# Kernel tuning notes

Hardware: AMD Instinct MI355X
Metric: run time of the kernel (lower is better)

The kernel has to match this reference:

```python
import jax, jax.numpy as jnp
import numpy as np

N_NODES = 50000
N_EDGES = 800000
EMB = 128
N_LAYERS = 2
BN_EPS = 1e-5


def setup_inputs() -> dict:
    key = jax.random.key(0)
    ks = jax.random.split(key, 16)
    N, E, D, L = N_NODES, N_EDGES, EMB, N_LAYERS
    x = jax.random.randint(ks[0], (N, 2), 0, 3)
    edge_index = jax.random.randint(ks[1], (2, E), 0, N)
    edge_attr = jax.random.randint(ks[2], (E, 2), 0, 3)
    batch = jnp.zeros((N,), dtype=jnp.int32)
    s = 0.1
    xemb1 = jax.random.normal(ks[3], (120, D)) * s   # atom-type embedding
    xemb2 = jax.random.normal(ks[4], (3, D)) * s     # chirality embedding
    e1 = jax.random.normal(ks[5], (L, 7, D)) * s     # bond-type embedding per layer
    e2 = jax.random.normal(ks[6], (L, 3, D)) * s     # bond-direction embedding per layer
    W1 = jax.random.normal(ks[7], (L, D, 2 * D)) * s
    b1 = jnp.zeros((L, 2 * D))
    W2 = jax.random.normal(ks[8], (L, 2 * D, D)) * s
    b2 = jnp.zeros((L, D))
    gamma = jnp.ones((L, D))
    beta = jnp.zeros((L, D))
    return {"x": x, "edge_index": edge_index, "edge_attr": edge_attr, "batch": batch,
            "xemb1": xemb1, "xemb2": xemb2, "e1": e1, "e2": e2,
            "W1": W1, "b1": b1, "W2": W2, "b2": b2, "gamma": gamma, "beta": beta}


def _gnn_forward(x, edge_index, edge_attr, xemb1, xemb2, e1, e2, W1, b1, W2, b2, gamma, beta):
    N = x.shape[0]
    # add self loops; self-loop edge_attr = [4, 0]
    loop = jnp.arange(N, dtype=edge_index.dtype)
    src = jnp.concatenate([edge_index[0], loop])
    dst = jnp.concatenate([edge_index[1], loop])
    loop_attr = jnp.concatenate([jnp.full((N, 1), 4, dtype=edge_attr.dtype),
                                 jnp.zeros((N, 1), dtype=edge_attr.dtype)], axis=1)
    ea = jnp.concatenate([edge_attr, loop_attr], axis=0)  # [E+N, 2]

    # input node embedding
    h = xemb1[x[:, 0]] + xemb2[x[:, 1]]  # [N, D]

    for l in range(N_LAYERS):
        eemb = e1[l][ea[:, 0]] + e2[l][ea[:, 1]]      # [E+N, D]
        msg = h[src] + eemb                            # gather + edge fuse
        agg = jax.ops.segment_sum(msg, dst, num_segments=N)  # scatter-add
        # GIN update MLP: Linear -> ReLU -> Linear
        h2 = jax.nn.relu(agg @ W1[l] + b1[l]) @ W2[l] + b2[l]
        # BatchNorm1d (training mode: biased batch stats)
        mu = jnp.mean(h2, axis=0)
        var = jnp.mean(jnp.square(h2 - mu), axis=0)
        h2 = gamma[l] * (h2 - mu) * jax.lax.rsqrt(var + BN_EPS) + beta[l]
        # dropout(relu) for non-final layers; drop_ratio=0 -> identity dropout
        h = h2 if l == N_LAYERS - 1 else jax.nn.relu(h2)
    return h  # JK='last'


def reference(x, edge_index, edge_attr, batch, xemb1, xemb2, e1, e2, W1, b1, W2, b2, gamma, beta):
    return _gnn_forward(x, edge_index, edge_attr, xemb1, xemb2, e1, e2, W1, b1, W2, b2, gamma, beta)
```

## Files before the change

kernel.cpp:

```cpp
#include <hip/hip_runtime.h>
#include <stdint.h>

#define N_NODES 50000
#define N_EDGES 800000
#define EMB 128
#define NPAD 50176
#define MBLK 392
#define BN_EPS 1e-5f
#define SENT_KEY ((N_NODES << 5) | 21)
#define NODES_PER_XCD 6250
#define XCHUNK 2048
#define NCHUNKS ((N_EDGES + XCHUNK - 1) / XCHUNK)
#define PBLK 196

typedef __attribute__((ext_vector_type(8))) short short8;
typedef __attribute__((ext_vector_type(4))) float f32x4;

__device__ __forceinline__ unsigned short f2bf(float f) {
    unsigned int u = __float_as_uint(f);
    u += 0x7fffu + ((u >> 16) & 1u);
    return (unsigned short)(u >> 16);
}
__device__ __forceinline__ float bflo(unsigned int v) { return __uint_as_float(v << 16); }
__device__ __forceinline__ float bfhi(unsigned int v) { return __uint_as_float(v & 0xffff0000u); }
__device__ __forceinline__ unsigned int packbf(float lo, float hi) {
    return (unsigned int)f2bf(lo) | ((unsigned int)f2bf(hi) << 16);
}

__global__ void k_prep(const int* __restrict__ x, const float* __restrict__ xe1,
                       const float* __restrict__ xe2, unsigned int* __restrict__ h,
                       const float* __restrict__ W1, const float* __restrict__ W2,
                       unsigned short* __restrict__ w1t, unsigned short* __restrict__ w2t,
                       int* __restrict__ deg,
                       const int* __restrict__ ei, const int* __restrict__ ea,
                       int* __restrict__ keyv, float* __restrict__ bnsum,
                       int* __restrict__ bmeta) {
    int idx = blockIdx.x * 256 + threadIdx.x;
    int i = idx >> 6, j = idx & 63;
    if (i < N_NODES) {
        int a = x[2 * i], c = x[2 * i + 1];
        float2 va = *(const float2*)(xe1 + a * EMB + j * 2);
        float2 vb = *(const float2*)(xe2 + c * EMB + j * 2);
        h[i * 64 + j] = packbf(va.x + vb.x, va.y + vb.y);
    } else if (i == N_NODES) {
        h[(size_t)i * 64 + j] = 0u;
    }
    if (idx < 4 * 32768) {
        int sec = idx >> 15, q = idx & 32767;
        if (sec < 2) {
            int r = q >> 8, c = q & 255;
            w1t[sec * 32768 + c * 128 + r] = f2bf(W1[sec * 32768 + q]);
        } else {
            int s = sec - 2;
            int r = q >> 7, c = q & 127;
            w2t[s * 32768 + c * 256 + r] = f2bf(W2[s * 32768 + q]);
        }
    }
    if (idx < N_EDGES) {
        int2 aa = *(const int2*)(ea + 2 * idx);
        keyv[idx] = (ei[idx] << 5) | (aa.x * 3 + aa.y);
    }
    if (idx < N_NODES) deg[idx] = 0;
    if (idx < 512) bnsum[idx] = 0.f;
    if (idx < 16) bmeta[idx] = 0;
}

__global__ void k_hist(const int* __restrict__ dst, int* __restrict__ deg) {
    int xcd = blockIdx.x & 7, chunk = blockIdx.x >> 3;
    int lo = xcd * NODES_PER_XCD, hi = lo + NODES_PER_XCD;
    int e0 = chunk * XCHUNK + threadIdx.x * 4;
#pragma unroll
    for (int it = 0; it < XCHUNK / 1024; ++it) {
        int e = e0 + it * 1024;
        if (e < N_EDGES) {
            int4 d4 = *(const int4*)(dst + e);
            if (d4.x >= lo && d4.x < hi) atomicAdd(&deg[d4.x], 1);
            if (d4.y >= lo && d4.y < hi) atomicAdd(&deg[d4.y], 1);
            if (d4.z >= lo && d4.z < hi) atomicAdd(&deg[d4.z], 1);
            if (d4.w >= lo && d4.w < hi) atomicAdd(&deg[d4.w], 1);
        }
    }
}

__global__ void k_scan1(const int* __restrict__ deg, int* __restrict__ part, int* __restrict__ bsums) {
    __shared__ int wsum[16];
    int lane = threadIdx.x & 63, wid = threadIdx.x >> 6;
    int i = blockIdx.x * 1024 + threadIdx.x;
    int d = (i < N_NODES) ? deg[i] : 0;
    int v = (d + 15) & ~15;
    int s = v;
#pragma unroll
    for (int off = 1; off < 64; off <<= 1) {
        int t = __shfl_up(s, off);
        if (lane >= off) s += t;
    }
    if (lane == 63) wsum[wid] = s;
    __syncthreads();
    if (wid == 0) {
        int w = (lane < 16) ? wsum[lane] : 0;
#pragma unroll
        for (int off = 1; off < 16; off <<= 1) {
            int t = __shfl_up(w, off);
            if (lane >= off) w += t;
        }
        if (lane < 16) wsum[lane] = w;
    }
    __syncthreads();
    int base = (wid > 0) ? wsum[wid - 1] : 0;
    if (i < N_NODES) part[i] = base + s - v;
    if (threadIdx.x == 1023) bsums[blockIdx.x] = wsum[15];
}

__global__ void k_scan3(const int* __restrict__ part, const int* __restrict__ bsums,
                        const int* __restrict__ deg, int* __restrict__ offs,
                        int* __restrict__ cursor, int* __restrict__ keys,
                        int* __restrict__ bcnt) {
    __shared__ int bs[64];
    __shared__ int lc[8];
    int tid = threadIdx.x;
    if (tid < 8) lc[tid] = 0;
    if (tid < 64) {
        int v = (tid < 49) ? bsums[tid] : 0;
        int orig = v;
#pragma unroll
        for (int off = 1; off < 64; off <<= 1) {
            int t = __shfl_up(v, off);
            if (tid >= off) v += t;
        }
        bs[tid] = v - orig;
    }
    __syncthreads();
    int i = blockIdx.x * 256 + tid;
    if (i < N_NODES) {
        int o = part[i] + bs[i >> 10];
        offs[i] = o;
        cursor[i] = o;
        int d = deg[i], pd = (d + 15) & ~15;
        for (int j = d; j < pd; ++j) keys[o + j] = SENT_KEY;
        if (i == N_NODES - 1) offs[N_NODES] = o + pd;
        int nch = pd >> 4;
        atomicAdd(&lc[nch > 7 ? 7 : nch], 1);
    }
    __syncthreads();
    if (tid < 8) atomicAdd(&bcnt[tid], lc[tid]);
}

__global__ void k_fill(const int* __restrict__ dst, const int* __restrict__ keyv,
                       int* __restrict__ cursor, int* __restrict__ keys,
                       const int* __restrict__ deg, const int* __restrict__ bcnt,
                       int* __restrict__ bcur, int* __restrict__ perm) {
    int xcd = blockIdx.x & 7, chunk = blockIdx.x >> 3;
    int lo = xcd * NODES_PER_XCD, hi = lo + NODES_PER_XCD;
    int e0 = chunk * XCHUNK + threadIdx.x * 4;
#pragma unroll
    for (int it = 0; it < XCHUNK / 1024; ++it) {
        int e = e0 + it * 1024;
        if (e < N_EDGES) {
            int4 d4 = *(const int4*)(dst + e);
            int dv[4] = {d4.x, d4.y, d4.z, d4.w};
#pragma unroll
            for (int q = 0; q < 4; ++q) {
                int d = dv[q];
                if (d >= lo && d < hi) {
                    int p = atomicAdd(&cursor[d], 1);
                    keys[p] = keyv[e + q];
                }
            }
        }
    }
    if (blockIdx.x < PBLK) {
        __shared__ int lcnt[8], gbase[8], tbase[8];
        if (threadIdx.x < 8) lcnt[threadIdx.x] = 0;
        __syncthreads();
        int i = blockIdx.x * 256 + threadIdx.x;
        int b = 0, lrank = 0;
        if (i < N_NODES) {
            int nch = (deg[i] + 15) >> 4;
            b = nch > 7 ? 7 : nch;
            lrank = atomicAdd(&lcnt[b], 1);
        }
        __syncthreads();
        if (threadIdx.x < 8) {
            gbase[threadIdx.x] = atomicAdd(&bcur[threadIdx.x], lcnt[threadIdx.x]);
            int s = 0;
            for (int k = 0; k < threadIdx.x; ++k) s += bcnt[k];
            tbase[threadIdx.x] = s;
        }
        __syncthreads();
        if (i < N_NODES) perm[tbase[b] + gbase[b] + lrank] = i;
    }
}

__global__ __launch_bounds__(256) void k_agg(
    const unsigned int* __restrict__ h,
    const int* __restrict__ offs,
    const int* __restrict__ keys,
    const int* __restrict__ perm,
    const float* __restrict__ e1l, const float* __restrict__ e2l,
    unsigned int* __restrict__ agg)
{
    __shared__ float e12[22 * 132];
    for (int t = threadIdx.x; t < 22 * 128; t += 256) {
        int combo = t >> 7, f = t & 127;
        float v = 0.f;
        if (combo < 21) {
            int a0 = combo / 3, a1 = combo - a0 * 3;
            v = e1l[a0 * EMB + f] + e2l[a1 * EMB + f];
        }
        e12[combo * 132 + f] = v;
    }
    __syncthreads();
    int wave = threadIdx.x >> 6, lane = threadIdx.x & 63;
    int sub = lane >> 4, fl = lane & 15;
    int slot = blockIdx.x * 16 + wave * 4 + sub;
    int node = (slot < N_NODES) ? perm[slot] : slot;
    float ax[8] = {0.f, 0.f, 0.f, 0.f, 0.f, 0.f, 0.f, 0.f};
    int o = 0, nch = 0;
    if (node < N_NODES) {
        o = offs[node];
        nch = (offs[node + 1] - o) >> 4;
        uint4 hv = *(const uint4*)(h + (size_t)node * 64 + fl * 4);
        const float* ep = e12 + 12 * 132 + fl * 8;
        float4 e0 = *(const float4*)ep, e1_ = *(const float4*)(ep + 4);
        ax[0] = bflo(hv.x) + e0.x;  ax[1] = bfhi(hv.x) + e0.y;
        ax[2] = bflo(hv.y) + e0.z;  ax[3] = bfhi(hv.y) + e0.w;
        ax[4] = bflo(hv.z) + e1_.x; ax[5] = bfhi(hv.z) + e1_.y;
        ax[6] = bflo(hv.w) + e1_.z; ax[7] = bfhi(hv.w) + e1_.w;
    }
    int maxch = nch;
#pragma unroll
    for (int d = 32; d; d >>= 1) maxch = max(maxch, __shfl_xor(maxch, d));
    int key = (0 < nch) ? keys[o + fl] : SENT_KEY;
    for (int c = 0; c < maxch; ++c) {
        int keyn = (c + 1 < nch) ? keys[o + (c + 1) * 16 + fl] : SENT_KEY;
#pragma unroll
        for (int j = 0; j < 16; ++j) {
            int kj = __shfl(key, sub * 16 + j);
            uint4 g = *(const uint4*)(h + (size_t)(kj >> 5) * 64 + fl * 4);
            const float* ep = e12 + (kj & 31) * 132 + fl * 8;
            float4 e0 = *(const float4*)ep, e1_ = *(const float4*)(ep + 4);
            ax[0] += bflo(g.x) + e0.x;  ax[1] += bfhi(g.x) + e0.y;
            ax[2] += bflo(g.y) + e0.z;  ax[3] += bfhi(g.y) + e0.w;
            ax[4] += bflo(g.z) + e1_.x; ax[5] += bfhi(g.z) + e1_.y;
            ax[6] += bflo(g.w) + e1_.z; ax[7] += bfhi(g.w) + e1_.w;
        }
        key = keyn;
    }
    {
        uint4 out;
        out.x = packbf(ax[0], ax[1]); out.y = packbf(ax[2], ax[3]);
        out.z = packbf(ax[4], ax[5]); out.w = packbf(ax[6], ax[7]);
        *(uint4*)(agg + (size_t)node * 64 + fl * 4) = out;
    }
}

__global__ __launch_bounds__(256, 2) void k_mlp(
    unsigned short* aggh2,
    const unsigned short* __restrict__ w1t,
    const float* __restrict__ b1,
    const unsigned short* __restrict__ w2t,
    const float* __restrict__ b2,
    float* __restrict__ bnsum)
{
    __shared__ float bn[256];
    int lane = threadIdx.x & 63;
    int wave = threadIdx.x >> 6;
    int quad = lane >> 4, r16 = lane & 15;
    int m0 = (blockIdx.x * 4 + wave) * 32;
    int sel  = (lane >> 5) & 1;
    int srcA = ((lane >> 4) & 1) * 32 + r16;
    int srcB = srcA + 16;
    bn[threadIdx.x] = 0.f;

    short8 bagg[2][4];
#pragma unroll
    for (int t = 0; t < 2; ++t)
#pragma unroll
        for (int c = 0; c < 4; ++c)
            bagg[t][c] = *(const short8*)(aggh2 + (size_t)(m0 + t * 16 + r16) * 128 + c * 32 + quad * 8);

    float b2v[8];
#pragma unroll
    for (int n = 0; n < 8; ++n) b2v[n] = b2[n * 16 + r16];

    f32x4 acc2[2][8];
#pragma unroll
    for (int t = 0; t < 2; ++t)
#pragma unroll
        for (int n = 0; n < 8; ++n) acc2[t][n] = (f32x4){0.f, 0.f, 0.f, 0.f};

    for (int c2 = 0; c2 < 8; ++c2) {
        unsigned int pk[2][2][2];
#pragma unroll
        for (int ntl = 0; ntl < 2; ++ntl) {
            int nt = c2 * 2 + ntl;
            short8 aw[4];
#pragma unroll
            for (int c = 0; c < 4; ++c)
                aw[c] = *(const short8*)(w1t + (nt * 16 + r16) * 128 + c * 32 + quad * 8);
            float4 bv = *(const float4*)(b1 + nt * 16 + quad * 4);
#pragma unroll
            for (int t = 0; t < 2; ++t) {
                f32x4 a1 = {0.f, 0.f, 0.f, 0.f};
#pragma unroll
                for (int c = 0; c < 4; ++c)
                    a1 = __builtin_amdgcn_mfma_f32_16x16x32_bf16(aw[c], bagg[t][c], a1, 0, 0, 0);
                float v0 = a1[0] + bv.x; v0 = v0 > 0.f ? v0 : 0.f;
                float v1 = a1[1] + bv.y; v1 = v1 > 0.f ? v1 : 0.f;
                float v2 = a1[2] + bv.z; v2 = v2 > 0.f ? v2 : 0.f;
                float v3 = a1[3] + bv.w; v3 = v3 > 0.f ? v3 : 0.f;
                pk[ntl][t][0] = packbf(v0, v1);
                pk[ntl][t][1] = packbf(v2, v3);
            }
        }
        short8 a2f[2];
#pragma unroll
        for (int t = 0; t < 2; ++t) {
            int u0 = __shfl((int)pk[0][t][0], srcA), w0 = __shfl((int)pk[1][t][0], srcA);
            int u1 = __shfl((int)pk[0][t][1], srcA), w1_ = __shfl((int)pk[1][t][1], srcA);
            int u2 = __shfl((int)pk[0][t][0], srcB), w2_ = __shfl((int)pk[1][t][0], srcB);
            int u3 = __shfl((int)pk[0][t][1], srcB), w3_ = __shfl((int)pk[1][t][1], srcB);
            union { int i[4]; short8 s; } a2u;
            a2u.i[0] = sel ? w0 : u0;
            a2u.i[1] = sel ? w1_ : u1;
            a2u.i[2] = sel ? w2_ : u2;
            a2u.i[3] = sel ? w3_ : u3;
            a2f[t] = a2u.s;
        }
#pragma unroll
        for (int n = 0; n < 8; ++n) {
            short8 bw = *(const short8*)(w2t + (n * 16 + r16) * 256 + c2 * 32 + quad * 8);
            acc2[0][n] = __builtin_amdgcn_mfma_f32_16x16x32_bf16(a2f[0], bw, acc2[0][n], 0, 0, 0);
            acc2[1][n] = __builtin_amdgcn_mfma_f32_16x16x32_bf16(a2f[1], bw, acc2[1][n], 0, 0, 0);
        }
    }
    float s[8], q[8];
#pragma unroll
    for (int n = 0; n < 8; ++n) { s[n] = 0.f; q[n] = 0.f; }
#pragma unroll
    for (int t = 0; t < 2; ++t)
#pragma unroll
        for (int n = 0; n < 8; ++n)
#pragma unroll
            for (int r = 0; r < 4; ++r) {
                int row = m0 + t * 16 + quad * 4 + r;
                float v = acc2[t][n][r] + b2v[n];
                if (row < N_NODES) {
                    aggh2[(size_t)row * 128 + n * 16 + r16] = f2bf(v);
                    s[n] += v; q[n] += v * v;
                }
            }
#pragma unroll
    for (int n = 0; n < 8; ++n) {
        s[n] += __shfl_xor(s[n], 16); q[n] += __shfl_xor(q[n], 16);
        s[n] += __shfl_xor(s[n], 32); q[n] += __shfl_xor(q[n], 32);
    }
    __syncthreads();
    if (quad == 0) {
#pragma unroll
        for (int n = 0; n < 8; ++n) {
            atomicAdd(&bn[n * 16 + r16], s[n]);
            atomicAdd(&bn[128 + n * 16 + r16], q[n]);
        }
    }
    __syncthreads();
    atomicAdd(&bnsum[threadIdx.x], bn[threadIdx.x]);
}

__global__ void k_bnnorm(const uint4* __restrict__ h2, const float* __restrict__ bnsum,
                         const float* __restrict__ gamma, const float* __restrict__ beta,
                         uint4* __restrict__ outb, float4* __restrict__ outf, int mode) {
    __shared__ float ab[256];
    int tid = threadIdx.x;
    if (tid < 128) {
        float mean = bnsum[tid] * (1.f / N_NODES);
        float var  = bnsum[128 + tid] * (1.f / N_NODES) - mean * mean;
        float rstd = rsqrtf(var + BN_EPS);
        float g = gamma[tid];
        ab[tid]       = g * rstd;
        ab[128 + tid] = beta[tid] - mean * g * rstd;
    }
    __syncthreads();
    int idx = blockIdx.x * 256 + tid;
    if (idx >= N_NODES * 16) return;
    int p = (idx & 15) * 8;
    uint4 hv = h2[idx];
    float v0 = bflo(hv.x) * ab[p + 0] + ab[128 + p + 0];
    float v1 = bfhi(hv.x) * ab[p + 1] + ab[128 + p + 1];
    float v2 = bflo(hv.y) * ab[p + 2] + ab[128 + p + 2];
    float v3 = bfhi(hv.y) * ab[p + 3] + ab[128 + p + 3];
    float v4 = bflo(hv.z) * ab[p + 4] + ab[128 + p + 4];
    float v5 = bfhi(hv.z) * ab[p + 5] + ab[128 + p + 5];
    float v6 = bflo(hv.w) * ab[p + 6] + ab[128 + p + 6];
    float v7 = bfhi(hv.w) * ab[p + 7] + ab[128 + p + 7];
    if (mode == 0) {
        v0 = v0 > 0.f ? v0 : 0.f; v1 = v1 > 0.f ? v1 : 0.f;
        v2 = v2 > 0.f ? v2 : 0.f; v3 = v3 > 0.f ? v3 : 0.f;
        v4 = v4 > 0.f ? v4 : 0.f; v5 = v5 > 0.f ? v5 : 0.f;
        v6 = v6 > 0.f ? v6 : 0.f; v7 = v7 > 0.f ? v7 : 0.f;
        uint4 out;
        out.x = packbf(v0, v1); out.y = packbf(v2, v3);
        out.z = packbf(v4, v5); out.w = packbf(v6, v7);
        outb[idx] = out;
    } else {
        outf[2 * idx]     = make_float4(v0, v1, v2, v3);
        outf[2 * idx + 1] = make_float4(v4, v5, v6, v7);
    }
}

extern "C" void kernel_launch(void* const* d_in, const int* in_sizes, int n_in,
                              void* d_out, int out_size, void* d_ws, size_t ws_size,
                              hipStream_t stream) {
    const int* x  = (const int*)d_in[0];
    const int* ei = (const int*)d_in[1];
    const int* ea = (const int*)d_in[2];
    const float* xe1 = (const float*)d_in[4];
    const float* xe2 = (const float*)d_in[5];
    const float* e1  = (const float*)d_in[6];
    const float* e2  = (const float*)d_in[7];
    const float* W1  = (const float*)d_in[8];
    const float* b1  = (const float*)d_in[9];
    const float* W2  = (const float*)d_in[10];
    const float* b2  = (const float*)d_in[11];
    const float* gm  = (const float*)d_in[12];
    const float* bt  = (const float*)d_in[13];

    char* ws = (char*)d_ws;
    size_t off = 0;
    auto take = [&](size_t bytes) -> char* {
        char* p = ws + off;
        off = (off + bytes + 255) & ~(size_t)255;
        return p;
    };
    unsigned int* h_buf = (unsigned int*)take((size_t)(N_NODES + 1) * 64 * 4);
    unsigned int* aggb  = (unsigned int*)take((size_t)NPAD * 64 * 4);
    unsigned short* w1t = (unsigned short*)take((size_t)2 * 32768 * 2);
    unsigned short* w2t = (unsigned short*)take((size_t)2 * 32768 * 2);
    int* deg    = (int*)take((size_t)N_NODES * 4);
    int* offs   = (int*)take((size_t)(N_NODES + 1) * 4);
    int* cursor = (int*)take((size_t)N_NODES * 4);
    int* keys   = (int*)take((size_t)(N_EDGES + N_NODES * 16) * 4);
    int* keyv   = (int*)take((size_t)N_EDGES * 4);
    int* bsums  = (int*)take(64 * 4);
    float* bnsum = (float*)take(512 * 4);
    int* bmeta  = (int*)take(16 * 4);
    int* perm   = (int*)take((size_t)N_NODES * 4);
    int* bcnt = bmeta, *bcur = bmeta + 8;

    k_prep<<<((N_NODES + 1) * 64 + 255) / 256, 256, 0, stream>>>(x, xe1, xe2, h_buf,
                                                                 W1, W2, w1t, w2t, deg,
                                                                 ei, ea, keyv, bnsum, bmeta);
    k_hist<<<8 * NCHUNKS, 256, 0, stream>>>(ei + N_EDGES, deg);
    k_scan1<<<49, 1024, 0, stream>>>(deg, offs, bsums);
    k_scan3<<<(N_NODES + 255) / 256, 256, 0, stream>>>(offs, bsums, deg, offs, cursor, keys, bcnt);
    k_fill<<<8 * NCHUNKS, 256, 0, stream>>>(ei + N_EDGES, keyv, cursor, keys,
                                            deg, bcnt, bcur, perm);

    for (int l = 0; l < 2; ++l) {
        k_agg<<<NPAD / 16, 256, 0, stream>>>(h_buf, offs, keys, perm,
                                             e1 + l * 896, e2 + l * 384, aggb);
        k_mlp<<<MBLK, 256, 0, stream>>>((unsigned short*)aggb, w1t + l * 32768, b1 + l * 256,
                                        w2t + l * 32768, b2 + l * 128, bnsum + l * 256);
        k_bnnorm<<<(N_NODES * 16 + 255) / 256, 256, 0, stream>>>((const uint4*)aggb, bnsum + l * 256,
                                                                 gm + l * 128, bt + l * 128,
                                                                 (uint4*)h_buf, (float4*)d_out, l);
    }
}
```

Before: 382.9 us.

## Software-pipeline gather loads and interleave node slots across blocks in k_agg

The inner 16-neighbor gather loop in k_agg is split into two half-batches. The loads for the second half are issued while the first half is being accumulated, so more memory requests are in flight per wave. The launch bounds now request 4 blocks per CU. The wave-to-slot mapping is also permuted so that degree-sorted nodes are spread across blocks, which balances the mix of heavy and light nodes per CU. The exchange is higher register pressure from the eight buffered uint4 loads, which could cause spills under the tighter occupancy bound.

```diff
diff --git a/kernel.cpp b/kernel.cpp
--- a/kernel.cpp
+++ b/kernel.cpp
@@ -191,7 +191,7 @@
     }
 }
 
-__global__ __launch_bounds__(256) void k_agg(
+__global__ __launch_bounds__(256, 4) void k_agg(
     const unsigned int* __restrict__ h,
     const int* __restrict__ offs,
     const int* __restrict__ keys,
@@ -212,7 +212,9 @@
     __syncthreads();
     int wave = threadIdx.x >> 6, lane = threadIdx.x & 63;
     int sub = lane >> 4, fl = lane & 15;
-    int slot = blockIdx.x * 16 + wave * 4 + sub;
+    int wi = blockIdx.x * 4 + wave;
+    int q = (wi & 255) * 49 + (wi >> 8);
+    int slot = q * 4 + sub;
     int node = (slot < N_NODES) ? perm[slot] : slot;
     float ax[8] = {0.f, 0.f, 0.f, 0.f, 0.f, 0.f, 0.f, 0.f};
     int o = 0, nch = 0;
@@ -233,16 +235,34 @@
     int key = (0 < nch) ? keys[o + fl] : SENT_KEY;
     for (int c = 0; c < maxch; ++c) {
         int keyn = (c + 1 < nch) ? keys[o + (c + 1) * 16 + fl] : SENT_KEY;
-#pragma unroll
-        for (int j = 0; j < 16; ++j) {
-            int kj = __shfl(key, sub * 16 + j);
-            uint4 g = *(const uint4*)(h + (size_t)(kj >> 5) * 64 + fl * 4);
-            const float* ep = e12 + (kj & 31) * 132 + fl * 8;
+        int kjA[8], kjB[8];
+        uint4 g[8];
+#pragma unroll
+        for (int j = 0; j < 8; ++j) {
+            kjA[j] = __shfl(key, sub * 16 + j);
+            g[j] = *(const uint4*)(h + (size_t)(kjA[j] >> 5) * 64 + fl * 4);
+        }
+#pragma unroll
+        for (int j = 0; j < 8; ++j) {
+            uint4 gg = g[j];
+            kjB[j] = __shfl(key, sub * 16 + 8 + j);
+            g[j] = *(const uint4*)(h + (size_t)(kjB[j] >> 5) * 64 + fl * 4);
+            const float* ep = e12 + (kjA[j] & 31) * 132 + fl * 8;
             float4 e0 = *(const float4*)ep, e1_ = *(const float4*)(ep + 4);
-            ax[0] += bflo(g.x) + e0.x;  ax[1] += bfhi(g.x) + e0.y;
-            ax[2] += bflo(g.y) + e0.z;  ax[3] += bfhi(g.y) + e0.w;
-            ax[4] += bflo(g.z) + e1_.x; ax[5] += bfhi(g.z) + e1_.y;
-            ax[6] += bflo(g.w) + e1_.z; ax[7] += bfhi(g.w) + e1_.w;
+            ax[0] += bflo(gg.x) + e0.x;  ax[1] += bfhi(gg.x) + e0.y;
+            ax[2] += bflo(gg.y) + e0.z;  ax[3] += bfhi(gg.y) + e0.w;
+            ax[4] += bflo(gg.z) + e1_.x; ax[5] += bfhi(gg.z) + e1_.y;
+            ax[6] += bflo(gg.w) + e1_.z; ax[7] += bfhi(gg.w) + e1_.w;
+        }
+#pragma unroll
+        for (int j = 0; j < 8; ++j) {
+            uint4 gg = g[j];
+            const float* ep = e12 + (kjB[j] & 31) * 132 + fl * 8;
+            float4 e0 = *(const float4*)ep, e1_ = *(const float4*)(ep + 4);
+            ax[0] += bflo(gg.x) + e0.x;  ax[1] += bfhi(gg.x) + e0.y;
+            ax[2] += bflo(gg.y) + e0.z;  ax[3] += bfhi(gg.y) + e0.w;
+            ax[4] += bflo(gg.z) + e1_.x; ax[5] += bfhi(gg.z) + e1_.y;
+            ax[6] += bflo(gg.w) + e1_.z; ax[7] += bfhi(gg.w) + e1_.w;
         }
         key = keyn;
     }
```

Result: faster. 373.7 us (-2.4%).
